# Performance work log

Measured on AMD Instinct MI355X. Metric: run time of the kernel, lower is better.

Reference implementation:

```python
import jax, jax.numpy as jnp
import numpy as np

E = 8           # num_local_experts
H = 1024        # hidden_size
F = 1024        # moe_ffn_hidden_size (per-half; fc1 out = 2*F due to GLU)
T = 16384       # total dispatched tokens
GLU_LINEAR_OFFSET = 1.0


def setup_inputs() -> dict:
    key = jax.random.key(0)
    ks = jax.random.split(key, 7)
    s1 = 1.0 / np.sqrt(H)
    s2 = 1.0 / np.sqrt(F)
    return {
        "hidden_states": jax.random.normal(ks[0], (T, H), jnp.float32),
        "tokens_per_expert": jnp.full((E,), T // E, dtype=jnp.int64),
        "probs": jax.random.uniform(ks[1], (T,), jnp.float32),
        # expert params; torch Linear W is [out,in], stored here as [in,out] (same math)
        "W1": jax.random.uniform(ks[2], (E, H, 2 * F), jnp.float32, -s1, s1),
        "b1": jax.random.uniform(ks[3], (E, 2 * F), jnp.float32, -s1, s1),
        "W2": jax.random.uniform(ks[4], (E, F, H), jnp.float32, -s2, s2),
        "b2": jax.random.uniform(ks[5], (E, H), jnp.float32, -s2, s2),
    }


def reference(hidden_states, tokens_per_expert, probs, W1, b1, W2, b2):
    # Tokens arrive grouped contiguously by expert with equal counts (as in
    # setup_inputs), so the split/loop/cat in the torch module is exactly a
    # reshape + grouped (batched) GEMM over the expert axis.
    e = W1.shape[0]
    t, h = hidden_states.shape
    x = hidden_states.reshape(e, t // e, h)            # [E, Tpe, H]
    p = probs.reshape(e, t // e)                       # [E, Tpe]
    # fc1 (gated)
    y = jnp.einsum('eth,ehf->etf', x, W1) + b1[:, None, :]  # [E, Tpe, 2F]
    gate, lin = jnp.split(y, 2, axis=-1)
    a = jax.nn.silu(gate) * (lin + GLU_LINEAR_OFFSET)       # [E, Tpe, F]
    a = a * p[..., None]                                    # per-token scale
    # fc2
    out = jnp.einsum('etf,efh->eth', a, W2) + b2[:, None, :]
    return out.reshape(t, h)
```

## Files before the change

### kernel.cpp

```cpp
#include <hip/hip_runtime.h>
#include <hip/hip_bf16.h>
#include <stdint.h>

#define T_TOK 16384
#define H_DIM 1024
#define F_DIM 1024
#define E_NUM 8
#define TPE   2048

typedef unsigned short u16;
typedef __attribute__((ext_vector_type(8))) short bf16x8;
typedef __attribute__((ext_vector_type(4))) float f32x4;
typedef __attribute__((ext_vector_type(8))) u16 u16x8;

__device__ __forceinline__ u16 f2bf(float x) {
  unsigned int u = __float_as_uint(x);
  u = (u + 0x7fffu + ((u >> 16) & 1u)) >> 16;
  return (u16)u;
}

#define GLD16(gp, lp)                                                          \
  __builtin_amdgcn_global_load_lds(                                            \
      (const __attribute__((address_space(1))) void*)(gp),                     \
      (__attribute__((address_space(3))) void*)(lp), 16, 0, 0)

__global__ __launch_bounds__(256) void cvt_f32_bf16(
    const float* __restrict__ src, u16* __restrict__ dst, int n8) {
  int stride = gridDim.x * blockDim.x;
  for (int i = blockIdx.x * blockDim.x + threadIdx.x; i < n8; i += stride) {
    const float4* s = (const float4*)(src + (size_t)i * 8);
    float4 a = s[0], b = s[1];
    u16x8 o;
    o[0] = f2bf(a.x); o[1] = f2bf(a.y); o[2] = f2bf(a.z); o[3] = f2bf(a.w);
    o[4] = f2bf(b.x); o[5] = f2bf(b.y); o[6] = f2bf(b.z); o[7] = f2bf(b.w);
    *(u16x8*)(dst + (size_t)i * 8) = o;
  }
}

__global__ __launch_bounds__(256) void transpose_cvt(
    const float* __restrict__ src, u16* __restrict__ dst, int R, int C) {
  __shared__ float tile[64][65];
  int nCt = C >> 6, nRt = R >> 6;
  int per = nCt * nRt;
  int b = blockIdx.x;
  int e = b / per;
  int r2 = b - e * per;
  int rt = r2 / nCt, ct = r2 - rt * nCt;
  const float* s = src + (size_t)e * R * C + (size_t)(rt << 6) * C + (ct << 6);
  int t = threadIdx.x;
  int lr = t >> 4, lc = (t & 15) << 2;
#pragma unroll
  for (int i = 0; i < 4; i++) {
    float4 v = *(const float4*)(s + (size_t)(lr + i * 16) * C + lc);
    tile[lr + i * 16][lc + 0] = v.x;
    tile[lr + i * 16][lc + 1] = v.y;
    tile[lr + i * 16][lc + 2] = v.z;
    tile[lr + i * 16][lc + 3] = v.w;
  }
  __syncthreads();
  u16* d = dst + (size_t)e * C * R + (size_t)(ct << 6) * R + (rt << 6);
  int orow = t >> 2, ok = (t & 3) << 4;
  u16x8 o0, o1;
#pragma unroll
  for (int i = 0; i < 8; i++) o0[i] = f2bf(tile[ok + i][orow]);
#pragma unroll
  for (int i = 0; i < 8; i++) o1[i] = f2bf(tile[ok + 8 + i][orow]);
  *(u16x8*)(d + (size_t)orow * R + ok) = o0;
  *(u16x8*)(d + (size_t)orow * R + ok + 8) = o1;
}

__global__ __launch_bounds__(512, 1) void gemm1_act(
    const u16* __restrict__ xbf, const u16* __restrict__ w1t,
    const float* __restrict__ b1, const float* __restrict__ probs,
    u16* __restrict__ abf) {
  __shared__ char sm[49152];
  const int tid = threadIdx.x;
  const int lane = tid & 63;
  const int wid = tid >> 6;
  const int wm = wid >> 2, wn = wid & 3;
  const int bid = blockIdx.x;
  const int e = bid >> 7;
  const int mt = (bid >> 3) & 15;
  const int ct = bid & 7;
  const int tokBase = e * TPE + mt * 128;
  const int c0 = ct * 128;

  const u16* ag[2]; char* al[2];
#pragma unroll
  for (int q = 0; q < 2; q++) {
    int lin = q * 8192 + wid * 1024 + lane * 16;
    int lg = lin ^ (((lin >> 7) & 7) << 4);
    int row = lg >> 7, kk = (lg & 127) >> 1;
    ag[q] = xbf + (size_t)(tokBase + row) * H_DIM + kk;
    al[q] = sm + lin;
  }
  const u16* bg[4]; char* bl[4];
#pragma unroll
  for (int q = 0; q < 4; q++) {
    int lin = q * 8192 + wid * 1024 + lane * 16;
    int lg = lin ^ (((lin >> 7) & 7) << 4);
    int nn = lg >> 7, kk = (lg & 127) >> 1;
    int col = ((((nn >> 5) & 1)) << 10) + c0 + ((nn >> 6) << 5) + (nn & 31);
    bg[q] = w1t + (size_t)(e * 2 * F_DIM + col) * H_DIM + kk;
    bl[q] = sm + 16384 + lin;
  }

  const int lrow = lane & 15, lkhi = lane >> 4;
  int aoff[4], boff[4], koff[2];
#pragma unroll
  for (int i = 0; i < 4; i++) aoff[i] = (wm * 64 + i * 16 + lrow) * 128;
#pragma unroll
  for (int j = 0; j < 4; j++) boff[j] = 16384 + (wn * 64 + j * 16 + lrow) * 128;
#pragma unroll
  for (int ks = 0; ks < 2; ks++)
    koff[ks] = ((ks << 6) | (lkhi << 4)) ^ ((lane & 7) << 4);

  f32x4 acc[4][4];
#pragma unroll
  for (int i = 0; i < 4; i++)
#pragma unroll
    for (int j = 0; j < 4; j++) acc[i][j] = f32x4{0.f, 0.f, 0.f, 0.f};

  for (int kt = 0; kt < H_DIM / 64; ++kt) {
    __syncthreads();
    GLD16(ag[0], al[0]); GLD16(ag[1], al[1]);
    GLD16(bg[0], bl[0]); GLD16(bg[1], bl[1]);
    GLD16(bg[2], bl[2]); GLD16(bg[3], bl[3]);
    asm volatile("s_waitcnt vmcnt(0)" ::: "memory");
    __syncthreads();
#pragma unroll
    for (int ks = 0; ks < 2; ++ks) {
      bf16x8 afr[4], bfr[4];
#pragma unroll
      for (int i = 0; i < 4; i++)
        afr[i] = *(const bf16x8*)(sm + aoff[i] + koff[ks]);
#pragma unroll
      for (int j = 0; j < 4; j++)
        bfr[j] = *(const bf16x8*)(sm + boff[j] + koff[ks]);
#pragma unroll
      for (int i = 0; i < 4; i++)
#pragma unroll
        for (int j = 0; j < 4; j++)
          acc[i][j] = __builtin_amdgcn_mfma_f32_16x16x32_bf16(
              afr[i], bfr[j], acc[i][j], 0, 0, 0);
    }
#pragma unroll
    for (int q = 0; q < 2; q++) ag[q] += 64;
#pragma unroll
    for (int q = 0; q < 4; q++) bg[q] += 64;
  }

#pragma unroll
  for (int jj = 0; jj < 2; ++jj) {
    int cf = c0 + wn * 32 + jj * 16 + lrow;
    float gb = b1[e * 2 * F_DIM + cf];
    float lb = b1[e * 2 * F_DIM + F_DIM + cf];
#pragma unroll
    for (int i = 0; i < 4; i++) {
      int trow = tokBase + wm * 64 + i * 16 + lkhi * 4;
#pragma unroll
      for (int r = 0; r < 4; r++) {
        float g = acc[i][jj][r] + gb;
        float l = acc[i][jj + 2][r] + lb + 1.0f;
        float p = probs[trow + r];
        float sig = 1.0f / (1.0f + __expf(-g));
        float av = g * sig * l * p;
        abf[(size_t)(trow + r) * F_DIM + cf] = f2bf(av);
      }
    }
  }
}

__global__ __launch_bounds__(512, 1) void gemm2(
    const u16* __restrict__ abf, const u16* __restrict__ w2t,
    const float* __restrict__ b2, float* __restrict__ out) {
  __shared__ char sm[49152];
  const int tid = threadIdx.x;
  const int lane = tid & 63;
  const int wid = tid >> 6;
  const int wm = wid >> 2, wn = wid & 3;
  const int bid = blockIdx.x;
  const int e = bid >> 6;
  const int mt = (bid >> 2) & 15;
  const int nt = bid & 3;
  const int tokBase = e * TPE + mt * 128;
  const int h0 = nt * 256;

  const u16* ag[2]; char* al[2];
#pragma unroll
  for (int q = 0; q < 2; q++) {
    int lin = q * 8192 + wid * 1024 + lane * 16;
    int lg = lin ^ (((lin >> 7) & 7) << 4);
    int row = lg >> 7, kk = (lg & 127) >> 1;
    ag[q] = abf + (size_t)(tokBase + row) * F_DIM + kk;
    al[q] = sm + lin;
  }
  const u16* bg[4]; char* bl[4];
#pragma unroll
  for (int q = 0; q < 4; q++) {
    int lin = q * 8192 + wid * 1024 + lane * 16;
    int lg = lin ^ (((lin >> 7) & 7) << 4);
    int nn = lg >> 7, kk = (lg & 127) >> 1;
    bg[q] = w2t + (size_t)(e * H_DIM + h0 + nn) * F_DIM + kk;
    bl[q] = sm + 16384 + lin;
  }

  const int lrow = lane & 15, lkhi = lane >> 4;
  int aoff[4], boff[4], koff[2];
#pragma unroll
  for (int i = 0; i < 4; i++) aoff[i] = (wm * 64 + i * 16 + lrow) * 128;
#pragma unroll
  for (int j = 0; j < 4; j++) boff[j] = 16384 + (wn * 64 + j * 16 + lrow) * 128;
#pragma unroll
  for (int ks = 0; ks < 2; ks++)
    koff[ks] = ((ks << 6) | (lkhi << 4)) ^ ((lane & 7) << 4);

  f32x4 acc[4][4];
#pragma unroll
  for (int i = 0; i < 4; i++)
#pragma unroll
    for (int j = 0; j < 4; j++) acc[i][j] = f32x4{0.f, 0.f, 0.f, 0.f};

  for (int kt = 0; kt < F_DIM / 64; ++kt) {
    __syncthreads();
    GLD16(ag[0], al[0]); GLD16(ag[1], al[1]);
    GLD16(bg[0], bl[0]); GLD16(bg[1], bl[1]);
    GLD16(bg[2], bl[2]); GLD16(bg[3], bl[3]);
    asm volatile("s_waitcnt vmcnt(0)" ::: "memory");
    __syncthreads();
#pragma unroll
    for (int ks = 0; ks < 2; ++ks) {
      bf16x8 afr[4], bfr[4];
#pragma unroll
      for (int i = 0; i < 4; i++)
        afr[i] = *(const bf16x8*)(sm + aoff[i] + koff[ks]);
#pragma unroll
      for (int j = 0; j < 4; j++)
        bfr[j] = *(const bf16x8*)(sm + boff[j] + koff[ks]);
#pragma unroll
      for (int i = 0; i < 4; i++)
#pragma unroll
        for (int j = 0; j < 4; j++)
          acc[i][j] = __builtin_amdgcn_mfma_f32_16x16x32_bf16(
              afr[i], bfr[j], acc[i][j], 0, 0, 0);
    }
#pragma unroll
    for (int q = 0; q < 2; q++) ag[q] += 64;
#pragma unroll
    for (int q = 0; q < 4; q++) bg[q] += 64;
  }

#pragma unroll
  for (int j = 0; j < 4; ++j) {
    int h = h0 + wn * 64 + j * 16 + lrow;
    float bb = b2[e * H_DIM + h];
#pragma unroll
    for (int i = 0; i < 4; i++) {
      int trow = tokBase + wm * 64 + i * 16 + lkhi * 4;
#pragma unroll
      for (int r = 0; r < 4; r++)
        out[(size_t)(trow + r) * H_DIM + h] = acc[i][j][r] + bb;
    }
  }
}

extern "C" void kernel_launch(void* const* d_in, const int* in_sizes, int n_in,
                              void* d_out, int out_size, void* d_ws,
                              size_t ws_size, hipStream_t stream) {
  const float* x     = (const float*)d_in[0];
  const float* probs = (const float*)d_in[2];
  const float* W1    = (const float*)d_in[3];
  const float* b1    = (const float*)d_in[4];
  const float* W2    = (const float*)d_in[5];
  const float* b2    = (const float*)d_in[6];
  float* out = (float*)d_out;

  if (ws_size < 117440512u) return;
  char* ws = (char*)d_ws;
  u16* xbf = (u16*)(ws);
  u16* w1t = (u16*)(ws + 33554432);
  u16* w2t = (u16*)(ws + 67108864);
  u16* abf = (u16*)(ws + 83886080);

  cvt_f32_bf16<<<2048, 256, 0, stream>>>(x, xbf, (T_TOK * H_DIM) / 8);
  transpose_cvt<<<E_NUM * (2 * F_DIM / 64) * (H_DIM / 64), 256, 0, stream>>>(
      W1, w1t, H_DIM, 2 * F_DIM);
  transpose_cvt<<<E_NUM * (H_DIM / 64) * (F_DIM / 64), 256, 0, stream>>>(
      W2, w2t, F_DIM, H_DIM);
  gemm1_act<<<E_NUM * (TPE / 128) * (F_DIM / 128), 512, 0, stream>>>(
      xbf, w1t, b1, probs, abf);
  gemm2<<<E_NUM * (TPE / 128) * (H_DIM / 256), 512, 0, stream>>>(
      abf, w2t, b2, out);
}
```

Before: 167.3 us.

## Pipeline GEMMs with 256-row tiles, double-buffered LDS, and a fused prep kernel

Replaces the single-buffered GEMM loops with an 8-phase, double-buffered pipeline (128 KB dynamic LDS, 256x128 tiles per block) that issues global-to-LDS prefetches while MFMAs run, using barriers and s_setprio to interleave. The block index now puts the expert in the low bits, and the three preprocessing kernels are merged into one launch. The aim is to hide memory latency, raise per-block data reuse and cut launch overhead. In exchange it uses more registers per thread, and with 512-thread blocks and 128 KB LDS there are fewer blocks (512 and 256), which may leave part of the 256 CUs idle.

```diff
diff --git a/kernel.cpp b/kernel.cpp
--- a/kernel.cpp
+++ b/kernel.cpp
@@ -24,30 +24,34 @@
       (const __attribute__((address_space(1))) void*)(gp),                     \
       (__attribute__((address_space(3))) void*)(lp), 16, 0, 0)
 
-__global__ __launch_bounds__(256) void cvt_f32_bf16(
-    const float* __restrict__ src, u16* __restrict__ dst, int n8) {
-  int stride = gridDim.x * blockDim.x;
-  for (int i = blockIdx.x * blockDim.x + threadIdx.x; i < n8; i += stride) {
-    const float4* s = (const float4*)(src + (size_t)i * 8);
-    float4 a = s[0], b = s[1];
-    u16x8 o;
-    o[0] = f2bf(a.x); o[1] = f2bf(a.y); o[2] = f2bf(a.z); o[3] = f2bf(a.w);
-    o[4] = f2bf(b.x); o[5] = f2bf(b.y); o[6] = f2bf(b.z); o[7] = f2bf(b.w);
-    *(u16x8*)(dst + (size_t)i * 8) = o;
-  }
-}
-
-__global__ __launch_bounds__(256) void transpose_cvt(
-    const float* __restrict__ src, u16* __restrict__ dst, int R, int C) {
+__global__ __launch_bounds__(256) void prep(
+    const float* __restrict__ x, const float* __restrict__ W1,
+    const float* __restrict__ W2, u16* __restrict__ xbf,
+    u16* __restrict__ w1t, u16* __restrict__ w2t) {
   __shared__ float tile[64][65];
+  const int b = blockIdx.x;
+  const int t = threadIdx.x;
+  if (b < 2048) {
+    const int n8 = (T_TOK * H_DIM) / 8;
+    for (int i = b * 256 + t; i < n8; i += 2048 * 256) {
+      const float4* s = (const float4*)(x + (size_t)i * 8);
+      float4 a = s[0], c = s[1];
+      u16x8 o;
+      o[0] = f2bf(a.x); o[1] = f2bf(a.y); o[2] = f2bf(a.z); o[3] = f2bf(a.w);
+      o[4] = f2bf(c.x); o[5] = f2bf(c.y); o[6] = f2bf(c.z); o[7] = f2bf(c.w);
+      *(u16x8*)(xbf + (size_t)i * 8) = o;
+    }
+    return;
+  }
+  const float* src; u16* dst; int R, C, id;
+  if (b < 6144) { src = W1; dst = w1t; R = H_DIM; C = 2 * F_DIM; id = b - 2048; }
+  else          { src = W2; dst = w2t; R = F_DIM; C = H_DIM;     id = b - 6144; }
   int nCt = C >> 6, nRt = R >> 6;
   int per = nCt * nRt;
-  int b = blockIdx.x;
-  int e = b / per;
-  int r2 = b - e * per;
+  int e = id / per;
+  int r2 = id - e * per;
   int rt = r2 / nCt, ct = r2 - rt * nCt;
   const float* s = src + (size_t)e * R * C + (size_t)(rt << 6) * C + (ct << 6);
-  int t = threadIdx.x;
   int lr = t >> 4, lc = (t & 15) << 2;
 #pragma unroll
   for (int i = 0; i < 4; i++) {
@@ -69,196 +73,189 @@
   *(u16x8*)(d + (size_t)orow * R + ok + 8) = o1;
 }
 
-__global__ __launch_bounds__(512, 1) void gemm1_act(
+
+#define DSA(b, mi)                                                             \
+  _Pragma("unroll") for (int m2_ = 0; m2_ < 2; ++m2_)                          \
+  _Pragma("unroll") for (int ks_ = 0; ks_ < 2; ++ks_)                          \
+      aF[m2_][ks_] = *(const bf16x8*)(sm + (b) * 32768 + aRowBase +            \
+                                      ((mi) * 2 + m2_) * 2048 + koff[ks_]);
+
+#define DSB(b)                                                                 \
+  _Pragma("unroll") for (int n_ = 0; n_ < 4; ++n_)                             \
+  _Pragma("unroll") for (int ks_ = 0; ks_ < 2; ++ks_)                          \
+      bF[n_][ks_] = *(const bf16x8*)(sm + 65536 + (b) * 32768 + bRowBase +     \
+                                     n_ * 2048 + koff[ks_]);
+
+#define MFMA16(mi)                                                             \
+  _Pragma("unroll") for (int m2_ = 0; m2_ < 2; ++m2_)                          \
+  _Pragma("unroll") for (int n_ = 0; n_ < 4; ++n_)                             \
+  _Pragma("unroll") for (int ks_ = 0; ks_ < 2; ++ks_)                          \
+      acc[(mi) * 2 + m2_][n_] = __builtin_amdgcn_mfma_f32_16x16x32_bf16(       \
+          aF[m2_][ks_], bF[n_][ks_], acc[(mi) * 2 + m2_][n_], 0, 0, 0);
+
+#define PF_A(db, q, d) GLD16(aP[q] + (d), sm + (db) * 32768 + (q) * 8192 + tid * 16)
+#define PF_B(db, q, d) GLD16(bP[q] + (d), sm + 65536 + (db) * 32768 + (q) * 8192 + tid * 16)
+
+#define PHASE(b, mi, PFC, WTC)                                                 \
+  do {                                                                         \
+    if ((mi) == 0) { DSB(b); }                                                 \
+    DSA(b, mi);                                                                \
+    PFC                                                                        \
+    WTC                                                                        \
+    __builtin_amdgcn_s_barrier();                                              \
+    asm volatile("s_waitcnt lgkmcnt(0)" ::: "memory");                         \
+    __builtin_amdgcn_sched_barrier(0);                                         \
+    __builtin_amdgcn_s_setprio(1);                                             \
+    MFMA16(mi);                                                                \
+    __builtin_amdgcn_s_setprio(0);                                             \
+    __builtin_amdgcn_s_barrier();                                              \
+  } while (0)
+
+#define KLOOP_BODY                                                             \
+         \
+  PF_B(0, 0, 0); PF_B(0, 1, 0); PF_B(0, 2, 0); PF_B(0, 3, 0);                  \
+  PF_A(0, 0, 0); PF_A(0, 1, 0); PF_A(0, 2, 0); PF_A(0, 3, 0);                  \
+  PF_B(1, 0, 64); PF_B(1, 1, 64); PF_B(1, 2, 64); PF_B(1, 3, 64);              \
+  asm volatile("s_waitcnt vmcnt(4)" ::: "memory");                             \
+  __builtin_amdgcn_s_barrier();                                                \
+  for (int it = 0; it < 7; ++it) {                                             \
+    PHASE(0, 0, PF_A(1, 0, 64); PF_A(1, 1, 64);, );                            \
+    PHASE(0, 1, PF_A(1, 2, 64); PF_A(1, 3, 64);, );                            \
+    PHASE(0, 2, PF_B(0, 0, 128); PF_B(0, 1, 128);, );                          \
+    PHASE(0, 3, PF_B(0, 2, 128); PF_B(0, 3, 128);,                             \
+          asm volatile("s_waitcnt vmcnt(4)" ::: "memory"););                   \
+    PHASE(1, 0, PF_A(0, 0, 128); PF_A(0, 1, 128);, );                          \
+    PHASE(1, 1, PF_A(0, 2, 128); PF_A(0, 3, 128);, );                          \
+    PHASE(1, 2, PF_B(1, 0, 192); PF_B(1, 1, 192);, );                          \
+    PHASE(1, 3, PF_B(1, 2, 192); PF_B(1, 3, 192);,                             \
+          asm volatile("s_waitcnt vmcnt(4)" ::: "memory"););                   \
+    _Pragma("unroll") for (int q_ = 0; q_ < 4; ++q_) {                         \
+      aP[q_] += 128; bP[q_] += 128;                                            \
+    }                                                                          \
+  }                                                                            \
+                   \
+  PHASE(0, 0, PF_A(1, 0, 64); PF_A(1, 1, 64);, );                              \
+  PHASE(0, 1, PF_A(1, 2, 64); PF_A(1, 3, 64);, );                              \
+  PHASE(0, 2, , );                                                             \
+  PHASE(0, 3, , asm volatile("s_waitcnt vmcnt(0)" ::: "memory"););             \
+  PHASE(1, 0, , );                                                             \
+  PHASE(1, 1, , );                                                             \
+  PHASE(1, 2, , );                                                             \
+  PHASE(1, 3, , );
+
+__global__ __launch_bounds__(512, 2) void gemm1_8p(
     const u16* __restrict__ xbf, const u16* __restrict__ w1t,
     const float* __restrict__ b1, const float* __restrict__ probs,
     u16* __restrict__ abf) {
-  __shared__ char sm[49152];
+  extern __shared__ char sm[];
   const int tid = threadIdx.x;
   const int lane = tid & 63;
   const int wid = tid >> 6;
   const int wm = wid >> 2, wn = wid & 3;
   const int bid = blockIdx.x;
-  const int e = bid >> 7;
-  const int mt = (bid >> 3) & 15;
-  const int ct = bid & 7;
-  const int tokBase = e * TPE + mt * 128;
+  const int e = bid & 7;
+  const int inner = bid >> 3;
+  const int mt = inner >> 3, ct = inner & 7;
+  const int tokBase = e * TPE + mt * 256;
   const int c0 = ct * 128;
-
-  const u16* ag[2]; char* al[2];
-#pragma unroll
-  for (int q = 0; q < 2; q++) {
-    int lin = q * 8192 + wid * 1024 + lane * 16;
+  const int lrow = lane & 15, lkhi = lane >> 4;
+
+  const u16* aP[4]; const u16* bP[4];
+#pragma unroll
+  for (int q = 0; q < 4; ++q) {
+    int lin = q * 8192 + tid * 16;
     int lg = lin ^ (((lin >> 7) & 7) << 4);
     int row = lg >> 7, kk = (lg & 127) >> 1;
-    ag[q] = xbf + (size_t)(tokBase + row) * H_DIM + kk;
-    al[q] = sm + lin;
-  }
-  const u16* bg[4]; char* bl[4];
-#pragma unroll
-  for (int q = 0; q < 4; q++) {
-    int lin = q * 8192 + wid * 1024 + lane * 16;
-    int lg = lin ^ (((lin >> 7) & 7) << 4);
-    int nn = lg >> 7, kk = (lg & 127) >> 1;
-    int col = ((((nn >> 5) & 1)) << 10) + c0 + ((nn >> 6) << 5) + (nn & 31);
-    bg[q] = w1t + (size_t)(e * 2 * F_DIM + col) * H_DIM + kk;
-    bl[q] = sm + 16384 + lin;
-  }
-
-  const int lrow = lane & 15, lkhi = lane >> 4;
-  int aoff[4], boff[4], koff[2];
-#pragma unroll
-  for (int i = 0; i < 4; i++) aoff[i] = (wm * 64 + i * 16 + lrow) * 128;
-#pragma unroll
-  for (int j = 0; j < 4; j++) boff[j] = 16384 + (wn * 64 + j * 16 + lrow) * 128;
-#pragma unroll
-  for (int ks = 0; ks < 2; ks++)
+    aP[q] = xbf + (size_t)(tokBase + row) * H_DIM + kk;
+    int col = (((row >> 5) & 1) << 10) + c0 + ((row >> 6) << 5) + (row & 31);
+    bP[q] = w1t + (size_t)(e * 2 * F_DIM + col) * H_DIM + kk;
+  }
+  const int aRowBase = (wm * 128 + lrow) * 128;
+  const int bRowBase = (wn * 64 + lrow) * 128;
+  int koff[2];
+#pragma unroll
+  for (int ks = 0; ks < 2; ++ks)
     koff[ks] = ((ks << 6) | (lkhi << 4)) ^ ((lane & 7) << 4);
 
-  f32x4 acc[4][4];
-#pragma unroll
-  for (int i = 0; i < 4; i++)
-#pragma unroll
-    for (int j = 0; j < 4; j++) acc[i][j] = f32x4{0.f, 0.f, 0.f, 0.f};
-
-  for (int kt = 0; kt < H_DIM / 64; ++kt) {
-    __syncthreads();
-    GLD16(ag[0], al[0]); GLD16(ag[1], al[1]);
-    GLD16(bg[0], bl[0]); GLD16(bg[1], bl[1]);
-    GLD16(bg[2], bl[2]); GLD16(bg[3], bl[3]);
-    asm volatile("s_waitcnt vmcnt(0)" ::: "memory");
-    __syncthreads();
-#pragma unroll
-    for (int ks = 0; ks < 2; ++ks) {
-      bf16x8 afr[4], bfr[4];
-#pragma unroll
-      for (int i = 0; i < 4; i++)
-        afr[i] = *(const bf16x8*)(sm + aoff[i] + koff[ks]);
-#pragma unroll
-      for (int j = 0; j < 4; j++)
-        bfr[j] = *(const bf16x8*)(sm + boff[j] + koff[ks]);
-#pragma unroll
-      for (int i = 0; i < 4; i++)
-#pragma unroll
-        for (int j = 0; j < 4; j++)
-          acc[i][j] = __builtin_amdgcn_mfma_f32_16x16x32_bf16(
-              afr[i], bfr[j], acc[i][j], 0, 0, 0);
-    }
-#pragma unroll
-    for (int q = 0; q < 2; q++) ag[q] += 64;
-#pragma unroll
-    for (int q = 0; q < 4; q++) bg[q] += 64;
-  }
-
-#pragma unroll
-  for (int jj = 0; jj < 2; ++jj) {
-    int cf = c0 + wn * 32 + jj * 16 + lrow;
+  f32x4 acc[8][4];
+#pragma unroll
+  for (int i = 0; i < 8; ++i)
+#pragma unroll
+    for (int j = 0; j < 4; ++j) acc[i][j] = f32x4{0.f, 0.f, 0.f, 0.f};
+  bf16x8 aF[2][2], bF[4][2];
+
+  KLOOP_BODY
+
+#pragma unroll
+  for (int j = 0; j < 2; ++j) {
+    int cf = c0 + wn * 32 + j * 16 + lrow;
     float gb = b1[e * 2 * F_DIM + cf];
     float lb = b1[e * 2 * F_DIM + F_DIM + cf];
 #pragma unroll
-    for (int i = 0; i < 4; i++) {
-      int trow = tokBase + wm * 64 + i * 16 + lkhi * 4;
-#pragma unroll
-      for (int r = 0; r < 4; r++) {
-        float g = acc[i][jj][r] + gb;
-        float l = acc[i][jj + 2][r] + lb + 1.0f;
+    for (int i = 0; i < 8; ++i) {
+      int trow = tokBase + wm * 128 + i * 16 + lkhi * 4;
+#pragma unroll
+      for (int r = 0; r < 4; ++r) {
+        float g = acc[i][j][r] + gb;
+        float l = acc[i][j + 2][r] + lb + 1.0f;
         float p = probs[trow + r];
         float sig = 1.0f / (1.0f + __expf(-g));
-        float av = g * sig * l * p;
-        abf[(size_t)(trow + r) * F_DIM + cf] = f2bf(av);
+        abf[(size_t)(trow + r) * F_DIM + cf] = f2bf(g * sig * l * p);
       }
     }
   }
 }
 
-__global__ __launch_bounds__(512, 1) void gemm2(
+__global__ __launch_bounds__(512, 2) void gemm2_8p(
     const u16* __restrict__ abf, const u16* __restrict__ w2t,
     const float* __restrict__ b2, float* __restrict__ out) {
-  __shared__ char sm[49152];
+  extern __shared__ char sm[];
   const int tid = threadIdx.x;
   const int lane = tid & 63;
   const int wid = tid >> 6;
   const int wm = wid >> 2, wn = wid & 3;
   const int bid = blockIdx.x;
-  const int e = bid >> 6;
-  const int mt = (bid >> 2) & 15;
-  const int nt = bid & 3;
-  const int tokBase = e * TPE + mt * 128;
+  const int e = bid & 7;
+  const int inner = bid >> 3;
+  const int mt = inner >> 2, nt = inner & 3;
+  const int tokBase = e * TPE + mt * 256;
   const int h0 = nt * 256;
-
-  const u16* ag[2]; char* al[2];
-#pragma unroll
-  for (int q = 0; q < 2; q++) {
-    int lin = q * 8192 + wid * 1024 + lane * 16;
+  const int lrow = lane & 15, lkhi = lane >> 4;
+
+  const u16* aP[4]; const u16* bP[4];
+#pragma unroll
+  for (int q = 0; q < 4; ++q) {
+    int lin = q * 8192 + tid * 16;
     int lg = lin ^ (((lin >> 7) & 7) << 4);
     int row = lg >> 7, kk = (lg & 127) >> 1;
-    ag[q] = abf + (size_t)(tokBase + row) * F_DIM + kk;
-    al[q] = sm + lin;
-  }
-  const u16* bg[4]; char* bl[4];
-#pragma unroll
-  for (int q = 0; q < 4; q++) {
-    int lin = q * 8192 + wid * 1024 + lane * 16;
-    int lg = lin ^ (((lin >> 7) & 7) << 4);
-    int nn = lg >> 7, kk = (lg & 127) >> 1;
-    bg[q] = w2t + (size_t)(e * H_DIM + h0 + nn) * F_DIM + kk;
-    bl[q] = sm + 16384 + lin;
-  }
-
-  const int lrow = lane & 15, lkhi = lane >> 4;
-  int aoff[4], boff[4], koff[2];
-#pragma unroll
-  for (int i = 0; i < 4; i++) aoff[i] = (wm * 64 + i * 16 + lrow) * 128;
-#pragma unroll
-  for (int j = 0; j < 4; j++) boff[j] = 16384 + (wn * 64 + j * 16 + lrow) * 128;
-#pragma unroll
-  for (int ks = 0; ks < 2; ks++)
+    aP[q] = abf + (size_t)(tokBase + row) * F_DIM + kk;
+    bP[q] = w2t + (size_t)(e * H_DIM + h0 + row) * F_DIM + kk;
+  }
+  const int aRowBase = (wm * 128 + lrow) * 128;
+  const int bRowBase = (wn * 64 + lrow) * 128;
+  int koff[2];
+#pragma unroll
+  for (int ks = 0; ks < 2; ++ks)
     koff[ks] = ((ks << 6) | (lkhi << 4)) ^ ((lane & 7) << 4);
 
-  f32x4 acc[4][4];
-#pragma unroll
-  for (int i = 0; i < 4; i++)
-#pragma unroll
-    for (int j = 0; j < 4; j++) acc[i][j] = f32x4{0.f, 0.f, 0.f, 0.f};
-
-  for (int kt = 0; kt < F_DIM / 64; ++kt) {
-    __syncthreads();
-    GLD16(ag[0], al[0]); GLD16(ag[1], al[1]);
-    GLD16(bg[0], bl[0]); GLD16(bg[1], bl[1]);
-    GLD16(bg[2], bl[2]); GLD16(bg[3], bl[3]);
-    asm volatile("s_waitcnt vmcnt(0)" ::: "memory");
-    __syncthreads();
-#pragma unroll
-    for (int ks = 0; ks < 2; ++ks) {
-      bf16x8 afr[4], bfr[4];
-#pragma unroll
-      for (int i = 0; i < 4; i++)
-        afr[i] = *(const bf16x8*)(sm + aoff[i] + koff[ks]);
-#pragma unroll
-      for (int j = 0; j < 4; j++)
-        bfr[j] = *(const bf16x8*)(sm + boff[j] + koff[ks]);
-#pragma unroll
-      for (int i = 0; i < 4; i++)
-#pragma unroll
-        for (int j = 0; j < 4; j++)
-          acc[i][j] = __builtin_amdgcn_mfma_f32_16x16x32_bf16(
-              afr[i], bfr[j], acc[i][j], 0, 0, 0);
-    }
-#pragma unroll
-    for (int q = 0; q < 2; q++) ag[q] += 64;
-#pragma unroll
-    for (int q = 0; q < 4; q++) bg[q] += 64;
-  }
+  f32x4 acc[8][4];
+#pragma unroll
+  for (int i = 0; i < 8; ++i)
+#pragma unroll
+    for (int j = 0; j < 4; ++j) acc[i][j] = f32x4{0.f, 0.f, 0.f, 0.f};
+  bf16x8 aF[2][2], bF[4][2];
+
+  KLOOP_BODY
 
 #pragma unroll
   for (int j = 0; j < 4; ++j) {
     int h = h0 + wn * 64 + j * 16 + lrow;
     float bb = b2[e * H_DIM + h];
 #pragma unroll
-    for (int i = 0; i < 4; i++) {
-      int trow = tokBase + wm * 64 + i * 16 + lkhi * 4;
-#pragma unroll
-      for (int r = 0; r < 4; r++)
+    for (int i = 0; i < 8; ++i) {
+      int trow = tokBase + wm * 128 + i * 16 + lkhi * 4;
+#pragma unroll
+      for (int r = 0; r < 4; ++r)
         out[(size_t)(trow + r) * H_DIM + h] = acc[i][j][r] + bb;
     }
   }
@@ -282,13 +279,12 @@
   u16* w2t = (u16*)(ws + 67108864);
   u16* abf = (u16*)(ws + 83886080);
 
-  cvt_f32_bf16<<<2048, 256, 0, stream>>>(x, xbf, (T_TOK * H_DIM) / 8);
-  transpose_cvt<<<E_NUM * (2 * F_DIM / 64) * (H_DIM / 64), 256, 0, stream>>>(
-      W1, w1t, H_DIM, 2 * F_DIM);
-  transpose_cvt<<<E_NUM * (H_DIM / 64) * (F_DIM / 64), 256, 0, stream>>>(
-      W2, w2t, F_DIM, H_DIM);
-  gemm1_act<<<E_NUM * (TPE / 128) * (F_DIM / 128), 512, 0, stream>>>(
-      xbf, w1t, b1, probs, abf);
-  gemm2<<<E_NUM * (TPE / 128) * (H_DIM / 256), 512, 0, stream>>>(
-      abf, w2t, b2, out);
-}
+  (void)hipFuncSetAttribute(reinterpret_cast<const void*>(gemm1_8p),
+                            hipFuncAttributeMaxDynamicSharedMemorySize, 131072);
+  (void)hipFuncSetAttribute(reinterpret_cast<const void*>(gemm2_8p),
+                            hipFuncAttributeMaxDynamicSharedMemorySize, 131072);
+
+  prep<<<8192, 256, 0, stream>>>(x, W1, W2, xbf, w1t, w2t);
+  gemm1_8p<<<E_NUM * 8 * 8, 512, 131072, stream>>>(xbf, w1t, b1, probs, abf);
+  gemm2_8p<<<E_NUM * 8 * 4, 512, 131072, stream>>>(abf, w2t, b2, out);
+}
```

Result: faster. 153.9 us (-8.0%).
